# Kernel tuning notes

Hardware: AMD Instinct MI355X
Metric: run time of the kernel (lower is better)

## Reference

```python
import jax, jax.numpy as jnp
import numpy as np
from jax import lax

N_MELS, PRENET, ENC, DEC, ARNN, ADIM, NFILT, K = 80, 256, 512, 1024, 1024, 128, 32, 31
B, T_ENC, T_DEC = 16, 256, 200
PAD = (K - 1) // 2


def setup_inputs() -> dict:
    ks = jax.random.split(jax.random.key(0), 18)
    p = lambda k, s: jax.random.normal(k, s, jnp.float32) * 0.05
    return {
        "memory": jax.random.normal(ks[0], (B, T_ENC, ENC), jnp.float32),
        "decoder_inputs": jax.random.normal(ks[1], (B, N_MELS, T_DEC), jnp.float32),
        "memory_lengths": jax.random.randint(ks[2], (B,), T_ENC // 2, T_ENC),
        "prenet_w1": p(ks[3], (PRENET, N_MELS)),
        "prenet_w2": p(ks[4], (PRENET, PRENET)),
        "attn_rnn_w_ih": p(ks[5], (4 * ARNN, PRENET + ENC)),
        "attn_rnn_w_hh": p(ks[6], (4 * ARNN, ARNN)),
        "attn_rnn_b": p(ks[7], (4 * ARNN,)),
        "dec_rnn_w_ih": p(ks[8], (4 * DEC, ARNN + ENC)),
        "dec_rnn_w_hh": p(ks[9], (4 * DEC, DEC)),
        "dec_rnn_b": p(ks[10], (4 * DEC,)),
        "proj_w": p(ks[11], (N_MELS, DEC + ENC)),
        "proj_b": p(ks[12], (N_MELS,)),
        "query_w": p(ks[13], (ADIM, ARNN)),
        "memory_w": p(ks[14], (ADIM, ENC)),
        "v_w": p(ks[15], (1, ADIM)),
        "loc_conv_w": p(ks[16], (NFILT, 2, K)),
        "loc_dense_w": p(ks[17], (ADIM, NFILT)),
    }


def _lstm(x, h, c, w_ih, w_hh, b):
    g = x @ w_ih.T + h @ w_hh.T + b  # combined b_ih + b_hh
    i, f, gg, o = jnp.split(g, 4, axis=-1)
    c2 = jax.nn.sigmoid(f) * c + jax.nn.sigmoid(i) * jnp.tanh(gg)
    return jax.nn.sigmoid(o) * jnp.tanh(c2), c2


def _forward(memory, decoder_inputs, memory_lengths, prenet_w1, prenet_w2,
             attn_rnn_w_ih, attn_rnn_w_hh, attn_rnn_b,
             dec_rnn_w_ih, dec_rnn_w_hh, dec_rnn_b,
             proj_w, proj_b, query_w, memory_w, v_w, loc_conv_w, loc_dense_w):
    # [B, n_mels, T] -> [T+1, B, n_mels] with zero go-frame prepended
    x = jnp.transpose(decoder_inputs, (2, 0, 1))
    x = jnp.concatenate([jnp.zeros((1, B, N_MELS), x.dtype), x], axis=0)
    # prenet: two Linears (no bias) + relu + dropout(p=0.5, training hardcoded True)
    dk = jax.random.split(jax.random.key(42), 2)
    for w, k in ((prenet_w1, dk[0]), (prenet_w2, dk[1])):
        x = jax.nn.relu(x @ w.T)
        keep = jax.random.bernoulli(k, 0.5, x.shape)
        x = jnp.where(keep, x * 2.0, jnp.zeros((), x.dtype))
    dec_ins = x[:T_DEC]  # loop consumes steps 0..T_DEC-1
    # literal source semantics: mask True where t < length, those scores set to -inf
    mask = jnp.arange(T_ENC)[None, :] < memory_lengths[:, None]
    pmem = memory @ memory_w.T  # [B, T_enc, ADIM], computed once

    def step(carry, dec_in):
        ah, ac, dh, dc, aw, awc, actx = carry
        ah, ac = _lstm(jnp.concatenate([dec_in, actx], -1), ah, ac,
                       attn_rnn_w_ih, attn_rnn_w_hh, attn_rnn_b)
        awcat = jnp.stack([aw, awc], axis=1)  # [B, 2, T_enc]
        loc = lax.conv_general_dilated(awcat, loc_conv_w, (1,), [(PAD, PAD)],
                                       dimension_numbers=("NCH", "OIH", "NCH"))
        loc = jnp.einsum("bct,ac->bta", loc, loc_dense_w)  # [B, T_enc, ADIM]
        s = jnp.clip((ah @ query_w.T)[:, None, :] + loc + pmem, -20.0, 20.0)
        scores = jnp.tanh(s) @ v_w[0]  # [B, T_enc]
        scores = jnp.where(mask, -jnp.inf, scores)
        aw = jax.nn.softmax(scores + 1e-8, axis=1)
        awc = awc + aw
        actx = jnp.einsum("bt,bte->be", aw, memory)  # [B, ENC]
        dh, dc = _lstm(jnp.concatenate([ah, actx], -1), dh, dc,
                       dec_rnn_w_ih, dec_rnn_w_hh, dec_rnn_b)
        mel = jnp.concatenate([dh, actx], -1) @ proj_w.T + proj_b
        return (ah, ac, dh, dc, aw, awc, actx), mel

    z = lambda d: jnp.zeros((B, d), memory.dtype)
    carry0 = (z(ARNN), z(ARNN), z(DEC), z(DEC), z(T_ENC), z(T_ENC), z(ENC))
    _, mels = lax.scan(step, carry0, dec_ins)  # [T_DEC, B, N_MELS]
    out = jnp.transpose(mels, (1, 0, 2)).reshape(B, -1, N_MELS)
    return jnp.transpose(out, (0, 2, 1))  # [B, N_MELS, T_DEC]


def reference(memory, decoder_inputs, memory_lengths, prenet_w1, prenet_w2,
              attn_rnn_w_ih, attn_rnn_w_hh, attn_rnn_b,
              dec_rnn_w_ih, dec_rnn_w_hh, dec_rnn_b,
              proj_w, proj_b, query_w, memory_w, v_w, loc_conv_w, loc_dense_w):
    return _forward(memory, decoder_inputs, memory_lengths, prenet_w1, prenet_w2,
                    attn_rnn_w_ih, attn_rnn_w_hh, attn_rnn_b,
                    dec_rnn_w_ih, dec_rnn_w_hh, dec_rnn_b,
                    proj_w, proj_b, query_w, memory_w, v_w, loc_conv_w, loc_dense_w)
```

## Files before the change

kernel.cpp:

```cpp
#include <hip/hip_runtime.h>
#include <cstdint>
#include <cstddef>

#define TPB 1024
#define NB  256

typedef float4 f4;
typedef float f32x4 __attribute__((ext_vector_type(4)));
typedef short short8 __attribute__((ext_vector_type(8)));
typedef unsigned long long u64;

#define O_SLOT   0
#define O_AH     4352
#define O_AC     20736
#define O_DH     37120
#define O_DC     53504
#define O_ACTX   69888
#define O_AW     86272
#define O_AWC    90368
#define O_XU     94464
#define O_DECFR  135424
#define O_PMEM   545024
#define O_LDWBF  1069312
#define O_CONVWT 1071360
#define ZERO_BYTES (O_DECFR * 4)

#define XU_PAR  40960

#define SWZ(n, k) ((k) ^ (((n) & 7) << 3))

__device__ __forceinline__ void tf2x32(uint32_t k0, uint32_t k1, uint32_t x0, uint32_t x1,
                                       uint32_t& o0, uint32_t& o1) {
  uint32_t ks2 = k0 ^ k1 ^ 0x1BD11BDAu;
  x0 += k0; x1 += k1;
#define TFR(r) { x0 += x1; x1 = (x1 << (r)) | (x1 >> (32 - (r))); x1 ^= x0; }
  TFR(13) TFR(15) TFR(26) TFR(6)
  x0 += k1;  x1 += ks2 + 1u;
  TFR(17) TFR(29) TFR(16) TFR(24)
  x0 += ks2; x1 += k0 + 2u;
  TFR(13) TFR(15) TFR(26) TFR(6)
  x0 += k0;  x1 += k1 + 3u;
  TFR(17) TFR(29) TFR(16) TFR(24)
  x0 += k1;  x1 += ks2 + 4u;
  TFR(13) TFR(15) TFR(26) TFR(6)
  x0 += ks2; x1 += k0 + 5u;
#undef TFR
  o0 = x0; o1 = x1;
}
__device__ __forceinline__ uint32_t tf_fold(uint32_t k0, uint32_t k1, uint32_t idx) {
  uint32_t a, b; tf2x32(k0, k1, 0u, idx, a, b); return a ^ b;
}

__device__ __forceinline__ unsigned short f2bf(float x) {
  uint32_t u = __float_as_uint(x);
  u += 0x7fffu + ((u >> 16) & 1u);
  return (unsigned short)(u >> 16);
}
__device__ __forceinline__ float dot4(f4 a, f4 b, float acc) {
  acc = fmaf(a.x, b.x, acc); acc = fmaf(a.y, b.y, acc);
  acc = fmaf(a.z, b.z, acc); acc = fmaf(a.w, b.w, acc);
  return acc;
}
__device__ __forceinline__ float dot_f4(const float* __restrict__ x, const float* __restrict__ w, int n4) {
  const f4* xv = (const f4*)x; const f4* wv = (const f4*)w;
  float s = 0.f;
#pragma unroll 8
  for (int k = 0; k < n4; ++k) s = dot4(xv[k], wv[k], s);
  return s;
}
__device__ __forceinline__ float sigm(float x) { return 1.f / (1.f + expf(-x)); }
__device__ __forceinline__ float wave_sum(float s) {
#pragma unroll
  for (int off = 32; off; off >>= 1) s += __shfl_xor(s, off, 64);
  return s;
}
__device__ __forceinline__ float wave_max(float s) {
#pragma unroll
  for (int off = 32; off; off >>= 1) s = fmaxf(s, __shfl_xor(s, off, 64));
  return s;
}

__device__ __forceinline__ f4 load_sc_f4(const float* p) {
  union { f4 v; u64 u[2]; } r;
  r.u[0] = __hip_atomic_load((const u64*)p,     __ATOMIC_RELAXED, __HIP_MEMORY_SCOPE_AGENT);
  r.u[1] = __hip_atomic_load((const u64*)p + 1, __ATOMIC_RELAXED, __HIP_MEMORY_SCOPE_AGENT);
  return r.v;
}
__device__ __forceinline__ short8 load_sc_s8(const unsigned short* p) {
  union { short8 v; u64 u[2]; } r;
  r.u[0] = __hip_atomic_load((const u64*)p,     __ATOMIC_RELAXED, __HIP_MEMORY_SCOPE_AGENT);
  r.u[1] = __hip_atomic_load((const u64*)p + 1, __ATOMIC_RELAXED, __HIP_MEMORY_SCOPE_AGENT);
  return r.v;
}

__device__ __forceinline__ void poll_ge(unsigned* p, unsigned epoch) {
  int spins = 0;
  while (__hip_atomic_load(p, __ATOMIC_RELAXED, __HIP_MEMORY_SCOPE_AGENT) < epoch) {
    __builtin_amdgcn_s_sleep(1);
    if (++spins >= (1 << 14)) {
      spins = 0;
      (void)__hip_atomic_load(p, __ATOMIC_ACQUIRE, __HIP_MEMORY_SCOPE_AGENT);
    }
  }
}

__device__ __forceinline__ void grid_sync(unsigned* slots, unsigned epoch, int tid, int bid) {
  unsigned* go = slots + NB * 16;
  __syncthreads();
  if (tid == 0) __builtin_amdgcn_fence(__ATOMIC_RELEASE, "agent");
  if (bid == 0) {
    if (tid < NB) {
      if (tid == 0)
        __hip_atomic_store(slots, epoch, __ATOMIC_RELAXED, __HIP_MEMORY_SCOPE_AGENT);
      poll_ge(slots + tid * 16, epoch);
    }
    __syncthreads();
    if (tid == 0)
      __hip_atomic_store(go, epoch, __ATOMIC_RELAXED, __HIP_MEMORY_SCOPE_AGENT);
  } else {
    if (tid == 0) {
      __hip_atomic_store(slots + bid * 16, epoch, __ATOMIC_RELAXED, __HIP_MEMORY_SCOPE_AGENT);
      poll_ge(go, epoch);
    }
    __syncthreads();
  }
}

__device__ __forceinline__ void project(int tid, int b,
    const float* __restrict__ dhb, const float* __restrict__ axb,
    const float* __restrict__ proj_w, const float* __restrict__ proj_b,
    float* __restrict__ out, int tout) {
  const int wid = tid >> 6, l = tid & 63;
  f4 xp[6];
#pragma unroll
  for (int c = 0; c < 6; ++c) {
    const int kf = l + 64 * c;
    const float* p = (c < 4) ? dhb + kf * 4 : axb + (kf - 256) * 4;
    xp[c] = load_sc_f4(p);
  }
#pragma unroll
  for (int mi = 0; mi < 5; ++mi) {
    const int m = wid * 5 + mi;
    const f4* wr = (const f4*)(proj_w + (size_t)m * 1536);
    float s = 0.f;
#pragma unroll
    for (int c = 0; c < 6; ++c) s = dot4(wr[l + 64 * c], xp[c], s);
    s = wave_sum(s);
    if (l == 0) out[(size_t)b * 16000 + m * 200 + tout] = s + proj_b[m];
  }
}

__global__ __launch_bounds__(TPB, 4) void decoder_persistent_kernel(
    const float* __restrict__ memory, const float* __restrict__ dec_inp,
    const int* __restrict__ mem_len,
    const float* __restrict__ pw1, const float* __restrict__ pw2,
    const float* __restrict__ a_wih, const float* __restrict__ a_whh, const float* __restrict__ a_b,
    const float* __restrict__ d_wih, const float* __restrict__ d_whh, const float* __restrict__ d_b,
    const float* __restrict__ proj_w, const float* __restrict__ proj_b,
    const float* __restrict__ query_w, const float* __restrict__ memory_w,
    const float* __restrict__ v_w, const float* __restrict__ conv_w, const float* __restrict__ ldw,
    float* __restrict__ out, float* __restrict__ wsf) {
  __shared__ __align__(16) unsigned short Wc_sh[16 * 2568];
  __shared__ __align__(16) unsigned short Wa_sh[16 * 1800];
  __shared__ __align__(16) float scr[4096];

  unsigned* slots = (unsigned*)wsf;
  const int tid = threadIdx.x;
  const int bid = blockIdx.x;
  const int jbase = bid * 4;
  unsigned epoch = 0;

  unsigned short* xU    = (unsigned short*)(wsf + O_XU);
  unsigned short* decfr = (unsigned short*)(wsf + O_DECFR);
  unsigned short* ldwbf = (unsigned short*)(wsf + O_LDWBF);
  float* convwt = wsf + O_CONVWT;
  float* pmem   = wsf + O_PMEM;

  {
    uint32_t d00, d01, d10, d11;
    tf2x32(0u, 42u, 0u, 0u, d00, d01);
    tf2x32(0u, 42u, 0u, 1u, d10, d11);
    const int s = tid >> 8, st = tid & 255;
    float* xin = scr + s * 336;
    float* h1  = scr + s * 336 + 80;
    for (int base = bid * 4; base < 3200; base += NB * 4) {
      const int task = base + s;
      const int tt = task >> 4, b = task & 15;
      if (st < 80) xin[st] = (tt == 0) ? 0.f : dec_inp[(size_t)b * 16000 + st * 200 + (tt - 1)];
      __syncthreads();
      float acc = 0.f;
      const float* w1r = pw1 + st * 80;
#pragma unroll 4
      for (int mm = 0; mm < 80; ++mm) acc = fmaf(xin[mm], w1r[mm], acc);
      acc = fmaxf(acc, 0.f);
      const uint32_t idx = (uint32_t)task * 256u + (uint32_t)st;
      acc = (tf_fold(d00, d01, idx) >> 31) ? 0.f : acc * 2.f;
      h1[st] = acc;
      __syncthreads();
      float acc2 = 0.f;
      const float* w2r = pw2 + st * 256;
#pragma unroll 4
      for (int pp = 0; pp < 256; ++pp) acc2 = fmaf(h1[pp], w2r[pp], acc2);
      acc2 = fmaxf(acc2, 0.f);
      acc2 = (tf_fold(d10, d11, idx) >> 31) ? 0.f : acc2 * 2.f;
      decfr[(size_t)tt * 4096 + (st >> 3) * 128 + b * 8 + (st & 7)] = f2bf(acc2);
      __syncthreads();
    }
  }
  {
    const int s = tid >> 7, st = tid & 127;
    for (int base = bid * 8; base < 4096; base += NB * 8) {
      const int task = base + s;
      pmem[(size_t)task * 128 + st] =
          dot_f4(memory + (size_t)task * 512, memory_w + (size_t)st * 512, 128);
    }
  }
  for (int n = 0; n < 16; ++n) {
    const int g = n & 3, jl = n >> 2;
    const int row = g * 1024 + jbase + jl;
    const float* wC1 = d_wih + (size_t)row * 1536;
    const float* wC2 = d_whh + (size_t)row * 1024;
    for (int k = tid; k < 2560; k += TPB) {
      float v;
      if (k < 512)       v = wC1[1024 + k];
      else if (k < 1536) v = wC1[k - 512];
      else               v = wC2[k - 1536];
      Wc_sh[n * 2568 + SWZ(n, k)] = f2bf(v);
    }
    const float* wA1 = a_wih + (size_t)row * 768;
    const float* wA2 = a_whh + (size_t)row * 1024;
    for (int k = tid; k < 1792; k += TPB)
      Wa_sh[n * 1800 + SWZ(n, k)] = f2bf(k < 768 ? wA1[k] : wA2[k - 768]);
  }
  if (bid == 0) for (int i = tid; i < 4096; i += TPB) ldwbf[i] = f2bf(ldw[i]);
  if (bid == 1) for (int i = tid; i < 1984; i += TPB) {
    const int o = i & 31, ck = i >> 5;
    convwt[ck * 32 + o] = conv_w[o * 62 + ck];
  }
  ++epoch; grid_sync(slots, epoch, tid, bid);

  for (int t = -1; t < 200; ++t) {
    if (t >= 0) {
      if (bid < 16) {
        const int b = bid;
        float* awst  = scr;
        float* q_s   = scr + 320;
        float* e_red = scr + 448;
        unsigned short* loc_s = (unsigned short*)(scr + 704);
        float* red8  = scr;
        float* awv_s = scr + 16;
        float* part  = scr + 144;
        if (tid < 320) {
          const int c2 = tid / 160, j = tid % 160, p = 113 + j;
          awst[c2 * 160 + j] = (p < 256) ? wsf[(c2 ? O_AWC : O_AW) + b * 256 + p] : 0.f;
        }
        __syncthreads();
        {
          const int ttl = tid >> 3, o0 = (tid & 7) * 4;
          float l0 = 0.f, l1 = 0.f, l2 = 0.f, l3 = 0.f;
#pragma unroll
          for (int c2 = 0; c2 < 2; ++c2) {
            const float* src = awst + c2 * 160 + ttl;
            const float* wp  = convwt + (c2 * 31) * 32 + o0;
#pragma unroll
            for (int k = 0; k < 31; ++k) {
              const float v = src[k];
              const f4 wv = *(const f4*)(wp + k * 32);
              l0 = fmaf(v, wv.x, l0); l1 = fmaf(v, wv.y, l1);
              l2 = fmaf(v, wv.z, l2); l3 = fmaf(v, wv.w, l3);
            }
          }
          unsigned short* lp = loc_s + ttl * 40 + o0;
          lp[0] = f2bf(l0); lp[1] = f2bf(l1); lp[2] = f2bf(l2); lp[3] = f2bf(l3);
        }
        {
          const int w = tid >> 6, l = tid & 63;
          f4 xq[4];
#pragma unroll
          for (int c = 0; c < 4; ++c)
            xq[c] = load_sc_f4(wsf + O_AH + b * 1024 + (l + 64 * c) * 4);
#pragma unroll
          for (int i = 0; i < 8; ++i) {
            const int a = w * 8 + i;
            const f4* wr = (const f4*)(query_w + (size_t)a * 1024);
            float s = 0.f;
#pragma unroll
            for (int c = 0; c < 4; ++c) s = dot4(wr[l + 64 * c], xq[c], s);
            s = wave_sum(s);
            if (l == 0) q_s[a] = s;
          }
        }
        __syncthreads();
        {
          const int w = tid >> 6, l = tid & 63, q = l >> 4, c = l & 15;
          const int ttile = w >> 1;
          const short8 af = *(const short8*)(loc_s + (ttile * 16 + c) * 40 + q * 8);
          float eacc[4] = {0.f, 0.f, 0.f, 0.f};
#pragma unroll
          for (int at = 0; at < 4; ++at) {
            const int a = ((w & 1) * 4 + at) * 16 + c;
            const short8 bf = *(const short8*)(ldwbf + a * 32 + q * 8);
            f32x4 d = {0.f, 0.f, 0.f, 0.f};
            d = __builtin_amdgcn_mfma_f32_16x16x32_bf16(af, bf, d, 0, 0, 0);
            const float qa = q_s[a];
            const float vv = v_w[a];
#pragma unroll
            for (int r = 0; r < 4; ++r) {
              const int tt = 128 + ttile * 16 + 4 * q + r;
              float s = d[r] + qa + pmem[(size_t)(b * 256 + tt) * 128 + a];
              s = fminf(20.f, fmaxf(-20.f, s));
              eacc[r] = fmaf(tanhf(s), vv, eacc[r]);
            }
          }
#pragma unroll
          for (int r = 0; r < 4; ++r) {
            float e = eacc[r];
            e += __shfl_xor(e, 1, 64); e += __shfl_xor(e, 2, 64);
            e += __shfl_xor(e, 4, 64); e += __shfl_xor(e, 8, 64);
            if (c == 0) e_red[(w & 1) * 128 + ttile * 16 + 4 * q + r] = e;
          }
        }
        __syncthreads();
        const int lenb = mem_len[b];
        float e = 0.f, p = 0.f; bool live = false;
        if (tid < 128) {
          const int tt = 128 + tid;
          live = tt >= lenb;
          e = e_red[tid] + e_red[128 + tid];
          float m = live ? e : -3.4e38f;
          m = wave_max(m);
          if ((tid & 63) == 0) red8[tid >> 6] = m;
        }
        __syncthreads();
        const float mx = fmaxf(red8[0], red8[1]);
        if (tid < 128) {
          p = live ? expf(e - mx) : 0.f;
          float z = wave_sum(p);
          if ((tid & 63) == 0) red8[2 + (tid >> 6)] = z;
        }
        __syncthreads();
        if (tid < 128) {
          const float z = red8[2] + red8[3];
          const float awv = live ? p / z : 0.f;
          awv_s[tid] = awv;
          wsf[O_AW + b * 256 + 128 + tid] = awv;
          if (live) wsf[O_AWC + b * 256 + 128 + tid] += awv;
        }
        __syncthreads();
        {
          const int th = tid >> 9, e0 = tid & 511;
          float a = 0.f;
#pragma unroll 4
          for (int j = 0; j < 64; ++j) {
            const int tt = 128 + th * 64 + j;
            a = fmaf(awv_s[th * 64 + j], memory[((size_t)(b * 256 + tt)) * 512 + e0], a);
          }
          part[th * 512 + e0] = a;
        }
        __syncthreads();
        if (tid < 512) {
          const float a = part[tid] + part[512 + tid];
          wsf[O_ACTX + (t & 1) * 8192 + b * 512 + tid] = a;
          xU[(t & 1) * XU_PAR + (tid >> 3) * 128 + b * 8 + (tid & 7)] = f2bf(a);
        }
      } else if (bid < 32 && t > 0) {
        const int b = bid - 16;
        project(tid, b, wsf + O_DH + b * 1024,
                wsf + O_ACTX + ((t - 1) & 1) * 8192 + b * 512, proj_w, proj_b, out, t - 1);
      }
      ++epoch; grid_sync(slots, epoch, tid, bid);
    }

    {
      const int rp = t & 1;
      const unsigned short* xUr = xU + rp * XU_PAR;
      unsigned short* xUw = xU + (rp ^ 1) * XU_PAR;
      float* redC = scr;
      float* redA = scr + 2048;
      const int w = tid >> 6, l = tid & 63;
      const int q = l >> 4, c = l & 15;
      if (w < 8) {
        if (t >= 0) {
          f32x4 acc = {0.f, 0.f, 0.f, 0.f};
#pragma unroll
          for (int i = 0; i < 10; ++i) {
            const int k32 = w * 10 + i;
            const short8 af = load_sc_s8(xUr + k32 * 512 + l * 8);
            const short8 bf = *(const short8*)(Wc_sh + c * 2568 + SWZ(c, q * 8 + k32 * 32));
            acc = __builtin_amdgcn_mfma_f32_16x16x32_bf16(af, bf, acc, 0, 0, 0);
          }
#pragma unroll
          for (int r = 0; r < 4; ++r) redC[w * 256 + (4 * q + r) * 16 + c] = acc[r];
        }
      } else {
        if (t < 199) {
          const unsigned short* dfr = decfr + (size_t)(t + 1) * 4096;
          f32x4 acc = {0.f, 0.f, 0.f, 0.f};
#pragma unroll
          for (int i = 0; i < 7; ++i) {
            const int k32 = (w - 8) * 7 + i;
            short8 af;
            if (k32 < 8) af = *(const short8*)(dfr + k32 * 512 + l * 8);
            else         af = load_sc_s8(xUr + (k32 - 8) * 512 + l * 8);
            const short8 bf = *(const short8*)(Wa_sh + c * 1800 + SWZ(c, q * 8 + k32 * 32));
            acc = __builtin_amdgcn_mfma_f32_16x16x32_bf16(af, bf, acc, 0, 0, 0);
          }
#pragma unroll
          for (int r = 0; r < 4; ++r) redA[(w - 8) * 256 + (4 * q + r) * 16 + c] = acc[r];
        }
      }
      __syncthreads();
      if (tid < 64) {
        if (t >= 0) {
          const int b = tid >> 2, jl = tid & 3, J = jbase + jl;
          float gv[4];
#pragma unroll
          for (int g = 0; g < 4; ++g) {
            float s = d_b[g * 1024 + J];
#pragma unroll
            for (int w2 = 0; w2 < 8; ++w2) s += redC[w2 * 256 + b * 16 + (jl * 4 + g)];
            gv[g] = s;
          }
          const int bi = b * 1024 + J;
          const float c2v = sigm(gv[1]) * wsf[O_DC + bi] + sigm(gv[0]) * tanhf(gv[2]);
          wsf[O_DC + bi] = c2v;
          const float h = sigm(gv[3]) * tanhf(c2v);
          wsf[O_DH + bi] = h;
          xUw[(192 + (J >> 3)) * 128 + b * 8 + (J & 7)] = f2bf(h);
        }
      } else if (tid < 128) {
        if (t < 199) {
          const int t2 = tid - 64;
          const int b = t2 >> 2, jl = t2 & 3, J = jbase + jl;
          float gv[4];
#pragma unroll
          for (int g = 0; g < 4; ++g) {
            float s = a_b[g * 1024 + J];
#pragma unroll
            for (int w2 = 0; w2 < 8; ++w2) s += redA[w2 * 256 + b * 16 + (jl * 4 + g)];
            gv[g] = s;
          }
          const int bi = b * 1024 + J;
          const float c2v = sigm(gv[1]) * wsf[O_AC + bi] + sigm(gv[0]) * tanhf(gv[2]);
          wsf[O_AC + bi] = c2v;
          const float h = sigm(gv[3]) * tanhf(c2v);
          wsf[O_AH + bi] = h;
          xUw[(64 + (J >> 3)) * 128 + b * 8 + (J & 7)] = f2bf(h);
        }
      }
    }
    ++epoch; grid_sync(slots, epoch, tid, bid);
  }

  if (bid >= 16 && bid < 32) {
    const int b = bid - 16;
    project(tid, b, wsf + O_DH + b * 1024, wsf + O_ACTX + 8192 + b * 512,
            proj_w, proj_b, out, 199);
  }
}

extern "C" void kernel_launch(void* const* d_in, const int* in_sizes, int n_in,
                              void* d_out, int out_size, void* d_ws, size_t ws_size,
                              hipStream_t stream) {
  (void)in_sizes; (void)n_in; (void)out_size; (void)ws_size;
  const float* memory   = (const float*)d_in[0];
  const float* dec_inp  = (const float*)d_in[1];
  const int*   mem_len  = (const int*)d_in[2];
  const float* pw1      = (const float*)d_in[3];
  const float* pw2      = (const float*)d_in[4];
  const float* a_wih    = (const float*)d_in[5];
  const float* a_whh    = (const float*)d_in[6];
  const float* a_b      = (const float*)d_in[7];
  const float* d_wih    = (const float*)d_in[8];
  const float* d_whh    = (const float*)d_in[9];
  const float* d_b      = (const float*)d_in[10];
  const float* proj_w   = (const float*)d_in[11];
  const float* proj_b   = (const float*)d_in[12];
  const float* query_w  = (const float*)d_in[13];
  const float* memory_w = (const float*)d_in[14];
  const float* v_w      = (const float*)d_in[15];
  const float* conv_w   = (const float*)d_in[16];
  const float* ldw      = (const float*)d_in[17];

  hipMemsetAsync(d_ws, 0, ZERO_BYTES, stream);
  decoder_persistent_kernel<<<NB, TPB, 0, stream>>>(
      memory, dec_inp, mem_len, pw1, pw2, a_wih, a_whh, a_b,
      d_wih, d_whh, d_b, proj_w, proj_b, query_w, memory_w, v_w, conv_w, ldw,
      (float*)d_out, (float*)d_ws);
}
```

Baseline: 16.02 ms.

## Replace mid-step grid barrier with partial barrier and drop release fences

The mid-step grid barrier, which follows the attention and projection phase, becomes a partial barrier. Only blocks 0-31 signal, and every block polls those 32 flags directly instead of routing through a master block. Shared state (actx, dh, ah, xU) is now written with agent-scope relaxed atomic stores, which lets the loop-end barrier skip its release fence. The bf16 hidden-state writes are packed four at a time through wave shuffles into 64-bit stores. The aim is to cut barrier latency on the serial 200-step recurrence, at the risk of memory-ordering bugs where the release fence was removed.

```diff
diff --git a/kernel.cpp b/kernel.cpp
--- a/kernel.cpp
+++ b/kernel.cpp
@@ -10,19 +10,20 @@
 typedef short short8 __attribute__((ext_vector_type(8)));
 typedef unsigned long long u64;
 
-#define O_SLOT   0
-#define O_AH     4352
-#define O_AC     20736
-#define O_DH     37120
-#define O_DC     53504
-#define O_ACTX   69888
-#define O_AW     86272
-#define O_AWC    90368
-#define O_XU     94464
-#define O_DECFR  135424
-#define O_PMEM   545024
-#define O_LDWBF  1069312
-#define O_CONVWT 1071360
+#define O_SLOTB  0
+#define O_SLOTA  4112
+#define O_AH     4864
+#define O_AC     21248
+#define O_DH     37632
+#define O_DC     54016
+#define O_ACTX   70400
+#define O_AW     86784
+#define O_AWC    90880
+#define O_XU     94976
+#define O_DECFR  135936
+#define O_PMEM   545536
+#define O_LDWBF  1069824
+#define O_CONVWT 1071872
 #define ZERO_BYTES (O_DECFR * 4)
 
 #define XU_PAR  40960
@@ -92,6 +93,12 @@
   r.u[1] = __hip_atomic_load((const u64*)p + 1, __ATOMIC_RELAXED, __HIP_MEMORY_SCOPE_AGENT);
   return r.v;
 }
+__device__ __forceinline__ void store_sc_f(float* p, float v) {
+  __hip_atomic_store(p, v, __ATOMIC_RELAXED, __HIP_MEMORY_SCOPE_AGENT);
+}
+__device__ __forceinline__ void store_sc_u64(u64* p, u64 v) {
+  __hip_atomic_store(p, v, __ATOMIC_RELAXED, __HIP_MEMORY_SCOPE_AGENT);
+}
 
 __device__ __forceinline__ void poll_ge(unsigned* p, unsigned epoch) {
   int spins = 0;
@@ -104,26 +111,35 @@
   }
 }
 
-__device__ __forceinline__ void grid_sync(unsigned* slots, unsigned epoch, int tid, int bid) {
-  unsigned* go = slots + NB * 16;
+__device__ __forceinline__ void grid_sync_full(unsigned* slotsB, unsigned ep, int tid, int bid,
+                                               bool fence) {
+  unsigned* go = slotsB + NB * 16;
   __syncthreads();
-  if (tid == 0) __builtin_amdgcn_fence(__ATOMIC_RELEASE, "agent");
+  if (fence && tid == 0) __builtin_amdgcn_fence(__ATOMIC_RELEASE, "agent");
   if (bid == 0) {
     if (tid < NB) {
       if (tid == 0)
-        __hip_atomic_store(slots, epoch, __ATOMIC_RELAXED, __HIP_MEMORY_SCOPE_AGENT);
-      poll_ge(slots + tid * 16, epoch);
+        __hip_atomic_store(slotsB, ep, __ATOMIC_RELAXED, __HIP_MEMORY_SCOPE_AGENT);
+      poll_ge(slotsB + tid * 16, ep);
     }
     __syncthreads();
     if (tid == 0)
-      __hip_atomic_store(go, epoch, __ATOMIC_RELAXED, __HIP_MEMORY_SCOPE_AGENT);
+      __hip_atomic_store(go, ep, __ATOMIC_RELAXED, __HIP_MEMORY_SCOPE_AGENT);
   } else {
     if (tid == 0) {
-      __hip_atomic_store(slots + bid * 16, epoch, __ATOMIC_RELAXED, __HIP_MEMORY_SCOPE_AGENT);
-      poll_ge(go, epoch);
+      __hip_atomic_store(slotsB + bid * 16, ep, __ATOMIC_RELAXED, __HIP_MEMORY_SCOPE_AGENT);
+      poll_ge(go, ep);
     }
     __syncthreads();
   }
+}
+
+__device__ __forceinline__ void grid_sync_partial(unsigned* slotsA, unsigned ep, int tid, int bid) {
+  __syncthreads();
+  if (bid < 32 && tid == 0)
+    __hip_atomic_store(slotsA + bid * 16, ep, __ATOMIC_RELAXED, __HIP_MEMORY_SCOPE_AGENT);
+  if (tid < 32) poll_ge(slotsA + tid * 16, ep);
+  __syncthreads();
 }
 
 __device__ __forceinline__ void project(int tid, int b,
@@ -164,11 +180,12 @@
   __shared__ __align__(16) unsigned short Wa_sh[16 * 1800];
   __shared__ __align__(16) float scr[4096];
 
-  unsigned* slots = (unsigned*)wsf;
+  unsigned* slotsB = (unsigned*)wsf;
+  unsigned* slotsA = (unsigned*)wsf + O_SLOTA;
   const int tid = threadIdx.x;
   const int bid = blockIdx.x;
   const int jbase = bid * 4;
-  unsigned epoch = 0;
+  unsigned ep1 = 0, ep2 = 0;
 
   unsigned short* xU    = (unsigned short*)(wsf + O_XU);
   unsigned short* decfr = (unsigned short*)(wsf + O_DECFR);
@@ -237,7 +254,7 @@
     const int o = i & 31, ck = i >> 5;
     convwt[ck * 32 + o] = conv_w[o * 62 + ck];
   }
-  ++epoch; grid_sync(slots, epoch, tid, bid);
+  ++ep2; grid_sync_full(slotsB, ep2, tid, bid, true);
 
   for (int t = -1; t < 200; ++t) {
     if (t >= 0) {
@@ -360,15 +377,26 @@
         __syncthreads();
         if (tid < 512) {
           const float a = part[tid] + part[512 + tid];
-          wsf[O_ACTX + (t & 1) * 8192 + b * 512 + tid] = a;
-          xU[(t & 1) * XU_PAR + (tid >> 3) * 128 + b * 8 + (tid & 7)] = f2bf(a);
+          store_sc_f(wsf + O_ACTX + (t & 1) * 8192 + b * 512 + tid, a);
+        }
+        if (tid < 64) {
+          u64 lo = 0, hi = 0;
+#pragma unroll
+          for (int e2 = 0; e2 < 4; ++e2)
+            lo |= (u64)f2bf(part[tid * 8 + e2] + part[512 + tid * 8 + e2]) << (16 * e2);
+#pragma unroll
+          for (int e2 = 4; e2 < 8; ++e2)
+            hi |= (u64)f2bf(part[tid * 8 + e2] + part[512 + tid * 8 + e2]) << (16 * (e2 - 4));
+          u64* dst = (u64*)(xU + (t & 1) * XU_PAR + tid * 128 + b * 8);
+          store_sc_u64(dst + 0, lo);
+          store_sc_u64(dst + 1, hi);
         }
       } else if (bid < 32 && t > 0) {
         const int b = bid - 16;
         project(tid, b, wsf + O_DH + b * 1024,
                 wsf + O_ACTX + ((t - 1) & 1) * 8192 + b * 512, proj_w, proj_b, out, t - 1);
       }
-      ++epoch; grid_sync(slots, epoch, tid, bid);
+      ++ep1; grid_sync_partial(slotsA, ep1, tid, bid);
     }
 
     {
@@ -425,8 +453,17 @@
           const float c2v = sigm(gv[1]) * wsf[O_DC + bi] + sigm(gv[0]) * tanhf(gv[2]);
           wsf[O_DC + bi] = c2v;
           const float h = sigm(gv[3]) * tanhf(c2v);
-          wsf[O_DH + bi] = h;
-          xUw[(192 + (J >> 3)) * 128 + b * 8 + (J & 7)] = f2bf(h);
+          store_sc_f(wsf + O_DH + bi, h);
+          const unsigned hb = f2bf(h);
+          const int lb = tid & ~3;
+          const unsigned v0 = __shfl(hb, lb + 0, 64);
+          const unsigned v1 = __shfl(hb, lb + 1, 64);
+          const unsigned v2 = __shfl(hb, lb + 2, 64);
+          const unsigned v3 = __shfl(hb, lb + 3, 64);
+          if (jl == 0) {
+            const u64 pk = (u64)v0 | ((u64)v1 << 16) | ((u64)v2 << 32) | ((u64)v3 << 48);
+            store_sc_u64((u64*)(xUw + (192 + (jbase >> 3)) * 128 + b * 8 + (jbase & 7)), pk);
+          }
         }
       } else if (tid < 128) {
         if (t < 199) {
@@ -444,12 +481,21 @@
           const float c2v = sigm(gv[1]) * wsf[O_AC + bi] + sigm(gv[0]) * tanhf(gv[2]);
           wsf[O_AC + bi] = c2v;
           const float h = sigm(gv[3]) * tanhf(c2v);
-          wsf[O_AH + bi] = h;
-          xUw[(64 + (J >> 3)) * 128 + b * 8 + (J & 7)] = f2bf(h);
+          store_sc_f(wsf + O_AH + bi, h);
+          const unsigned hb = f2bf(h);
+          const int lb = t2 & ~3;
+          const unsigned v0 = __shfl(hb, lb + 0, 64);
+          const unsigned v1 = __shfl(hb, lb + 1, 64);
+          const unsigned v2 = __shfl(hb, lb + 2, 64);
+          const unsigned v3 = __shfl(hb, lb + 3, 64);
+          if (jl == 0) {
+            const u64 pk = (u64)v0 | ((u64)v1 << 16) | ((u64)v2 << 32) | ((u64)v3 << 48);
+            store_sc_u64((u64*)(xUw + (64 + (jbase >> 3)) * 128 + b * 8 + (jbase & 7)), pk);
+          }
         }
       }
     }
-    ++epoch; grid_sync(slots, epoch, tid, bid);
+    ++ep2; grid_sync_full(slotsB, ep2, tid, bid, false);
   }
 
   if (bid >= 16 && bid < 32) {
```

After: 14.36 ms. 10.3% less time.
